# Kernel tuning notes

Hardware: AMD Instinct MI355X
Metric: run time of the kernel (lower is better)

Reference implementation:

```python
import jax, jax.numpy as jnp
import numpy as np

PAD = 3            # ConstantPad1d padding
PAD_VAL = -1.0     # ConstantPad1d value
STRIDE = 1
POOL = 2           # pool_size == pool_stride == 2
BN_EPS = 1e-5


def setup_inputs() -> dict:
    key = jax.random.key(0)
    k1, k2 = jax.random.split(key)
    x = jax.random.normal(k1, (256, 64, 4096), dtype=jnp.float32)
    W = jax.random.normal(k2, (128, 64, 7), dtype=jnp.float32)
    alpha = jnp.ones((1,), dtype=jnp.float32) * 0.25   # nn.PReLU default init
    gamma = jnp.ones((128,), dtype=jnp.float32)
    beta = jnp.zeros((128,), dtype=jnp.float32)
    return {"x": x, "W": W, "alpha": alpha, "gamma": gamma, "beta": beta}


def reference(x, W, alpha, gamma, beta):
    # 1) constant pad with value PAD_VAL along length
    xp = jnp.pad(x, ((0, 0), (0, 0), (PAD, PAD)), constant_values=PAD_VAL)
    # 2) binarize activations and weights (sign; sign(0)=0 as in torch)
    ba = jnp.sign(xp)
    bw = jnp.sign(W)
    # 3) float conv1d on +/-1 values, no bias  -> [B, Cout, L]
    y = jax.lax.conv_general_dilated(
        ba, bw, window_strides=(STRIDE,), padding='VALID',
        dimension_numbers=('NCW', 'OIW', 'NCW'))
    # 4) max pool k=2, s=2 (non-overlapping -> reshape trick)
    B, C, L = y.shape
    y = y[:, :, : (L // POOL) * POOL].reshape(B, C, L // POOL, POOL).max(axis=-1)
    # 5) PReLU with single shared alpha
    y = jnp.where(y > 0, y, alpha[0] * y)
    # 6) BatchNorm1d in training mode: batch stats over (B, L), biased variance
    mean = jnp.mean(y, axis=(0, 2), keepdims=True)
    var = jnp.mean((y - mean) ** 2, axis=(0, 2), keepdims=True)
    y = (y - mean) * jax.lax.rsqrt(var + BN_EPS)
    y = y * gamma[None, :, None] + beta[None, :, None]
    return y
```

## Files before the change

### kernel.cpp

```cpp
#include <hip/hip_runtime.h>
#include <stdint.h>

#define BATCH 256
#define CIN   64
#define LIN   4096
#define PADN  3
#define LPAD  4102
#define COUT  128
#define KW    7
#define LPOOL 2048
#define NBUCKET 64
#define NPERCH (256LL * 2048LL)

typedef unsigned long long u64;
typedef __attribute__((ext_vector_type(4)))  int i32x4;
typedef __attribute__((ext_vector_type(16))) int i32x16;
typedef __attribute__((ext_vector_type(8)))  short s16x8;

#define ACC_ZERO {0,0,0,0,0,0,0,0,0,0,0,0,0,0,0,0}

__global__ __launch_bounds__(256) void pack_x_kernel(const float* __restrict__ x,
                                                     char* __restrict__ sx,
                                                     int b_base)
{
    const int t  = threadIdx.x;
    const int lt = blockIdx.x;
    const int bl = blockIdx.y;
    const int b  = b_base + bl;
    const int l  = lt * 256 + t;
    const float* xb = x + (size_t)b * CIN * LIN + l;

    int o[16];
    #pragma unroll
    for (int cw = 0; cw < 16; ++cw) {
        unsigned wv = 0;
        #pragma unroll
        for (int j = 0; j < 4; ++j) {
            float v = xb[(size_t)(cw * 4 + j) * LIN];
            unsigned s = (v > 0.0f) ? 1u : ((v < 0.0f) ? 0xFFu : 0u);
            wv |= s << (8 * j);
        }
        o[cw] = (int)wv;
    }
    i32x4* dst = (i32x4*)(sx + ((size_t)bl * LPAD + (l + PADN)) * 64);
    dst[0] = (i32x4){o[0],  o[1],  o[2],  o[3]};
    dst[1] = (i32x4){o[4],  o[5],  o[6],  o[7]};
    dst[2] = (i32x4){o[8],  o[9],  o[10], o[11]};
    dst[3] = (i32x4){o[12], o[13], o[14], o[15]};

    const i32x4 ff = (i32x4){-1, -1, -1, -1};
    if (lt == 0 && t < PADN) {
        i32x4* pd = (i32x4*)(sx + ((size_t)bl * LPAD + t) * 64);
        pd[0] = ff; pd[1] = ff; pd[2] = ff; pd[3] = ff;
    }
    if (lt == 15 && t < PADN) {
        i32x4* pd = (i32x4*)(sx + ((size_t)bl * LPAD + (LIN + PADN) + t) * 64);
        pd[0] = ff; pd[1] = ff; pd[2] = ff; pd[3] = ff;
    }
}

__global__ __launch_bounds__(256) void pack_w_kernel(const float* __restrict__ w,
                                                     char* __restrict__ pwb)
{
    int idx = blockIdx.x * 256 + threadIdx.x;
    if (idx >= KW * COUT * CIN) return;
    int kk = idx >> 13;
    int co = (idx >> 6) & 127;
    int c  = idx & 63;
    float v = w[((size_t)co * CIN + c) * KW + kk];
    pwb[idx] = (char)((v > 0.0f) ? 1 : ((v < 0.0f) ? -1 : 0));
}

template<int STOREP>
__global__ __launch_bounds__(256, 3) void conv_stats_kernel(
    const char* __restrict__ sx, const char* __restrict__ pwb,
    u64* __restrict__ stats, short* __restrict__ pstore, int b_base)
{
    const int tid  = threadIdx.x;
    const int lane = tid & 63;
    const int w    = tid >> 6;
    const int ngrp = w & 1;
    const int mgrp = w >> 1;
    const int col  = lane & 31;
    const int hi   = lane >> 5;
    const int bl   = blockIdx.y;
    const int mchunk = blockIdx.x;

    const char* sxb = sx + (size_t)bl * LPAD * 64;
    const char* wb0 = pwb + (size_t)((ngrp * 64 + col) * 64) + hi * 16;

    const int gb = b_base + bl;
    short* prow0 = STOREP ? (pstore + ((size_t)gb * COUT + ngrp * 64 + col) * LPOOL)
                          : (short*)nullptr;
    short* prow1 = STOREP ? (prow0 + (size_t)32 * LPOOL) : (short*)nullptr;

    int sp0=0, sn0=0, qp0=0, qn0=0, sp1=0, sn1=0, qp1=0, qn1=0;

    for (int mt = 0; mt < 4; ++mt) {
        const int q0 = mchunk * 256 + mgrp * 128 + mt * 32;
        i32x16 acc0 = ACC_ZERO, acc1 = ACC_ZERO;
        #pragma unroll
        for (int kk = 0; kk < KW; ++kk) {
            const char* ar = sxb + (size_t)(q0 + col + kk) * 64;
            i32x4 x0 = *(const i32x4*)(ar + hi * 16);
            i32x4 x1 = *(const i32x4*)(ar + 32 + hi * 16);
            const char* wk = wb0 + (size_t)kk * (COUT * 64);
            i32x4 w00 = *(const i32x4*)(wk);
            i32x4 w01 = *(const i32x4*)(wk + 32);
            i32x4 w10 = *(const i32x4*)(wk + 2048);
            i32x4 w11 = *(const i32x4*)(wk + 2048 + 32);
            acc0 = __builtin_amdgcn_mfma_i32_32x32x32_i8(x0, w00, acc0, 0, 0, 0);
            acc0 = __builtin_amdgcn_mfma_i32_32x32x32_i8(x1, w01, acc0, 0, 0, 0);
            acc1 = __builtin_amdgcn_mfma_i32_32x32x32_i8(x0, w10, acc1, 0, 0, 0);
            acc1 = __builtin_amdgcn_mfma_i32_32x32x32_i8(x1, w11, acc1, 0, 0, 0);
        }
        const int lp0 = q0 >> 1;
        #pragma unroll
        for (int r = 0; r < 8; ++r) {
            int p = acc0[2*r] > acc0[2*r+1] ? acc0[2*r] : acc0[2*r+1];
            int q = p * p;
            bool pos = p > 0;
            sp0 += pos ? p : 0;  sn0 += pos ? 0 : p;
            qp0 += pos ? q : 0;  qn0 += pos ? 0 : q;
            int p1 = acc1[2*r] > acc1[2*r+1] ? acc1[2*r] : acc1[2*r+1];
            int q1 = p1 * p1;
            bool pos1 = p1 > 0;
            sp1 += pos1 ? p1 : 0;  sn1 += pos1 ? 0 : p1;
            qp1 += pos1 ? q1 : 0;  qn1 += pos1 ? 0 : q1;
            if (STOREP) {
                const int prow = (r & 1) + 4 * (r >> 1) + 2 * hi;
                prow0[lp0 + prow] = (short)p;
                prow1[lp0 + prow] = (short)p1;
            }
        }
    }

    sp0 += __shfl_xor(sp0, 32);  sn0 += __shfl_xor(sn0, 32);
    qp0 += __shfl_xor(qp0, 32);  qn0 += __shfl_xor(qn0, 32);
    sp1 += __shfl_xor(sp1, 32);  sn1 += __shfl_xor(sn1, 32);
    qp1 += __shfl_xor(qp1, 32);  qn1 += __shfl_xor(qn1, 32);

    if (hi == 0) {
        const int bkt = gb & (NBUCKET - 1);
        u64* s0 = stats + (size_t)(bkt * COUT + ngrp * 64 + col) * 4;
        atomicAdd(&s0[0], (u64)(long long)sp0);
        atomicAdd(&s0[1], (u64)(long long)sn0);
        atomicAdd(&s0[2], (u64)(long long)qp0);
        atomicAdd(&s0[3], (u64)(long long)qn0);
        u64* s1 = stats + (size_t)(bkt * COUT + ngrp * 64 + 32 + col) * 4;
        atomicAdd(&s1[0], (u64)(long long)sp1);
        atomicAdd(&s1[1], (u64)(long long)sn1);
        atomicAdd(&s1[2], (u64)(long long)qp1);
        atomicAdd(&s1[3], (u64)(long long)qn1);
    }
}

__global__ void finalize_kernel(const u64* __restrict__ stats,
                                const float* __restrict__ alpha,
                                const float* __restrict__ gamma,
                                const float* __restrict__ beta,
                                float2* __restrict__ scsh)
{
    int c = threadIdx.x;
    if (c >= COUT) return;
    long long s[4] = {0, 0, 0, 0};
    for (int bk = 0; bk < NBUCKET; ++bk)
        #pragma unroll
        for (int i = 0; i < 4; ++i)
            s[i] += (long long)stats[(size_t)(bk * COUT + c) * 4 + i];
    double a    = (double)alpha[0];
    double N    = (double)NPERCH;
    double sum  = (double)s[0] + a * (double)s[1];
    double ssq  = (double)s[2] + a * a * (double)s[3];
    double mean = sum / N;
    double var  = ssq / N - mean * mean;
    double inv  = 1.0 / sqrt(var + 1e-5);
    double g    = (double)gamma[c];
    scsh[c] = make_float2((float)(g * inv),
                          (float)((double)beta[c] - mean * g * inv));
}

__global__ __launch_bounds__(256) void bn_write_kernel(
    const short* __restrict__ p, const float2* __restrict__ scsh,
    const float* __restrict__ alpha, float* __restrict__ out)
{
    const float a = alpha[0];
    const size_t i = ((size_t)blockIdx.x * 256 + threadIdx.x) * 8;
    const int co = (int)((i >> 11) & (COUT - 1));
    const float2 ss = scsh[co];
    const s16x8 v = *(const s16x8*)(p + i);
    float4 o0, o1;
    #pragma unroll
    for (int j = 0; j < 4; ++j) {
        float pv = (float)v[j];
        float y = (pv > 0.0f) ? pv : a * pv;
        ((float*)&o0)[j] = fmaf(y, ss.x, ss.y);
    }
    #pragma unroll
    for (int j = 0; j < 4; ++j) {
        float pv = (float)v[4 + j];
        float y = (pv > 0.0f) ? pv : a * pv;
        ((float*)&o1)[j] = fmaf(y, ss.x, ss.y);
    }
    *(float4*)(out + i)     = o0;
    *(float4*)(out + i + 4) = o1;
}

__global__ __launch_bounds__(256, 2) void conv_write_kernel(
    const char* __restrict__ sx, const char* __restrict__ pwb,
    const float2* __restrict__ scsh, const float* __restrict__ alpha,
    float* __restrict__ out, int b_base)
{
    const int tid  = threadIdx.x;
    const int lane = tid & 63;
    const int w    = tid >> 6;
    const int ngrp = w & 1;
    const int mgrp = w >> 1;
    const int col  = lane & 31;
    const int hi   = lane >> 5;
    const int bl   = blockIdx.y;
    const int mchunk = blockIdx.x;

    const char* sxb = sx + (size_t)bl * LPAD * 64;
    const char* wb0 = pwb + (size_t)((ngrp * 64 + col) * 64) + hi * 16;

    const float a = alpha[0];
    const float2 ss0 = scsh[ngrp * 64 + col];
    const float2 ss1 = scsh[ngrp * 64 + 32 + col];
    const int gb = b_base + bl;
    float* orow0 = out + ((size_t)gb * COUT + ngrp * 64 + col) * LPOOL;
    float* orow1 = orow0 + (size_t)32 * LPOOL;

    for (int mt = 0; mt < 4; ++mt) {
        const int q0 = mchunk * 256 + mgrp * 128 + mt * 32;
        i32x16 a00 = ACC_ZERO, a01 = ACC_ZERO, a10 = ACC_ZERO, a11 = ACC_ZERO;
        #pragma unroll
        for (int kk = 0; kk < KW; ++kk) {
            const char* ar = sxb + (size_t)(q0 + col + kk) * 64;
            i32x4 x0 = *(const i32x4*)(ar + hi * 16);
            i32x4 x1 = *(const i32x4*)(ar + 32 + hi * 16);
            const char* wk = wb0 + (size_t)kk * (COUT * 64);
            i32x4 w00 = *(const i32x4*)(wk);
            i32x4 w01 = *(const i32x4*)(wk + 32);
            i32x4 w10 = *(const i32x4*)(wk + 2048);
            i32x4 w11 = *(const i32x4*)(wk + 2048 + 32);
            a00 = __builtin_amdgcn_mfma_i32_32x32x32_i8(x0, w00, a00, 0, 0, 0);
            a01 = __builtin_amdgcn_mfma_i32_32x32x32_i8(x1, w01, a01, 0, 0, 0);
            a10 = __builtin_amdgcn_mfma_i32_32x32x32_i8(x0, w10, a10, 0, 0, 0);
            a11 = __builtin_amdgcn_mfma_i32_32x32x32_i8(x1, w11, a11, 0, 0, 0);
        }
        i32x16 acc0 = a00 + a01;
        i32x16 acc1 = a10 + a11;
        const int lp0 = q0 >> 1;
        #pragma unroll
        for (int r = 0; r < 8; ++r) {
            const int prow = (r & 1) + 4 * (r >> 1) + 2 * hi;
            int p = acc0[2*r] > acc0[2*r+1] ? acc0[2*r] : acc0[2*r+1];
            float y = (p > 0) ? (float)p : a * (float)p;
            orow0[lp0 + prow] = fmaf(y, ss0.x, ss0.y);
            p = acc1[2*r] > acc1[2*r+1] ? acc1[2*r] : acc1[2*r+1];
            y = (p > 0) ? (float)p : a * (float)p;
            orow1[lp0 + prow] = fmaf(y, ss1.x, ss1.y);
        }
    }
}

extern "C" void kernel_launch(void* const* d_in, const int* in_sizes, int n_in,
                              void* d_out, int out_size, void* d_ws, size_t ws_size,
                              hipStream_t stream)
{
    const float* x     = (const float*)d_in[0];
    const float* W     = (const float*)d_in[1];
    const float* alpha = (const float*)d_in[2];
    const float* gamma = (const float*)d_in[3];
    const float* beta  = (const float*)d_in[4];
    float* out = (float*)d_out;

    const size_t sx_sz    = (size_t)BATCH * LPAD * 64;
    const size_t p_sz     = (size_t)BATCH * COUT * LPOOL * 2;
    const size_t pwb_sz   = (size_t)KW * COUT * CIN;
    const size_t stats_sz = (size_t)NBUCKET * COUT * 4 * 8;
    const size_t scsh_sz  = (size_t)COUT * 8;
    const size_t fixed    = pwb_sz + stats_sz + scsh_sz + 4096;

    char* ws = (char*)d_ws;

    if (ws_size >= sx_sz + p_sz + fixed) {
        char* sx = ws;
        size_t off = (sx_sz + 255) & ~(size_t)255;
        short* p = (short*)(ws + off);       off = (off + p_sz + 255) & ~(size_t)255;
        char* pwb = ws + off;                off = (off + pwb_sz + 255) & ~(size_t)255;
        u64* stats = (u64*)(ws + off);       off = (off + stats_sz + 255) & ~(size_t)255;
        float2* scsh = (float2*)(ws + off);

        hipMemsetAsync(stats, 0, stats_sz, stream);
        pack_w_kernel<<<dim3(224), 256, 0, stream>>>(W, pwb);
        pack_x_kernel<<<dim3(16, BATCH), 256, 0, stream>>>(x, sx, 0);
        conv_stats_kernel<1><<<dim3(16, BATCH), 256, 0, stream>>>(sx, pwb, stats, p, 0);
        finalize_kernel<<<dim3(1), 128, 0, stream>>>(stats, alpha, gamma, beta, scsh);
        bn_write_kernel<<<dim3(32768), 256, 0, stream>>>(p, scsh, alpha, out);
        return;
    }

    const size_t PER_B = (size_t)LPAD * 64;
    int nb = BATCH;
    if (ws_size < PER_B * BATCH + fixed) {
        size_t avail = (ws_size > fixed) ? (ws_size - fixed) : PER_B;
        nb = (int)(avail / PER_B);
        if (nb < 1) nb = 1;
        if (nb > BATCH) nb = BATCH;
    }

    char* sx = ws;
    size_t off = ((PER_B * (size_t)nb) + 255) & ~(size_t)255;
    char* pwb = ws + off;               off = (off + pwb_sz + 255) & ~(size_t)255;
    u64* stats = (u64*)(ws + off);      off = (off + stats_sz + 255) & ~(size_t)255;
    float2* scsh = (float2*)(ws + off);

    hipMemsetAsync(stats, 0, stats_sz, stream);
    pack_w_kernel<<<dim3(224), 256, 0, stream>>>(W, pwb);

    for (int b0 = 0; b0 < BATCH; b0 += nb) {
        int n = (BATCH - b0 < nb) ? (BATCH - b0) : nb;
        pack_x_kernel<<<dim3(16, n), 256, 0, stream>>>(x, sx, b0);
        conv_stats_kernel<0><<<dim3(16, n), 256, 0, stream>>>(sx, pwb, stats, nullptr, b0);
    }
    finalize_kernel<<<dim3(1), 128, 0, stream>>>(stats, alpha, gamma, beta, scsh);

    if (nb == BATCH) {
        conv_write_kernel<<<dim3(16, BATCH), 256, 0, stream>>>(sx, pwb, scsh, alpha, out, 0);
    } else {
        for (int b0 = 0; b0 < BATCH; b0 += nb) {
            int n = (BATCH - b0 < nb) ? (BATCH - b0) : nb;
            pack_x_kernel<<<dim3(16, n), 256, 0, stream>>>(x, sx, b0);
            conv_write_kernel<<<dim3(16, n), 256, 0, stream>>>(sx, pwb, scsh, alpha, out, b0);
        }
    }
}
```

Before: 388.4 us.

## Store pooled conv tiles in MFMA-native layout with vectorized packed writes

The stats kernel previously scattered 2-byte short stores into a row-major [B,Cout,L] intermediate, giving poorly coalesced writes. It now packs each lane's eight pooled values into one 16-byte store, laid out in per-wave MFMA fragment order. The BN write kernel is restructured to read that tiled layout, rebuild the logical positions and emit float4 output rows. This costs more complex indexing in the consumer, and its reads and writes may be less contiguous per thread.

```diff
diff --git a/kernel.cpp b/kernel.cpp
--- a/kernel.cpp
+++ b/kernel.cpp
@@ -19,6 +19,11 @@
 
 #define ACC_ZERO {0,0,0,0,0,0,0,0,0,0,0,0,0,0,0,0}
 
+static __device__ __forceinline__ int pk16(int a, int b)
+{
+    return (a & 0xFFFF) | (b << 16);
+}
+
 __global__ __launch_bounds__(256) void pack_x_kernel(const float* __restrict__ x,
                                                      char* __restrict__ sx,
                                                      int b_base)
@@ -90,9 +95,9 @@
     const char* wb0 = pwb + (size_t)((ngrp * 64 + col) * 64) + hi * 16;
 
     const int gb = b_base + bl;
-    short* prow0 = STOREP ? (pstore + ((size_t)gb * COUT + ngrp * 64 + col) * LPOOL)
-                          : (short*)nullptr;
-    short* prow1 = STOREP ? (prow0 + (size_t)32 * LPOOL) : (short*)nullptr;
+    short* pwave = STOREP
+        ? (pstore + ((((size_t)gb * 16 + mchunk) * 4 + w) * 2) * 4 * 64 * 8)
+        : (short*)nullptr;
 
     int sp0=0, sn0=0, qp0=0, qn0=0, sp1=0, sn1=0, qp1=0, qn1=0;
 
@@ -114,24 +119,32 @@
             acc1 = __builtin_amdgcn_mfma_i32_32x32x32_i8(x0, w10, acc1, 0, 0, 0);
             acc1 = __builtin_amdgcn_mfma_i32_32x32x32_i8(x1, w11, acc1, 0, 0, 0);
         }
-        const int lp0 = q0 >> 1;
+
+        int v0[8], v1[8];
         #pragma unroll
         for (int r = 0; r < 8; ++r) {
-            int p = acc0[2*r] > acc0[2*r+1] ? acc0[2*r] : acc0[2*r+1];
-            int q = p * p;
+            v0[r] = acc0[2*r] > acc0[2*r+1] ? acc0[2*r] : acc0[2*r+1];
+            v1[r] = acc1[2*r] > acc1[2*r+1] ? acc1[2*r] : acc1[2*r+1];
+        }
+        #pragma unroll
+        for (int r = 0; r < 8; ++r) {
+            int p = v0[r], q = p * p;
             bool pos = p > 0;
             sp0 += pos ? p : 0;  sn0 += pos ? 0 : p;
             qp0 += pos ? q : 0;  qn0 += pos ? 0 : q;
-            int p1 = acc1[2*r] > acc1[2*r+1] ? acc1[2*r] : acc1[2*r+1];
-            int q1 = p1 * p1;
+            int p1 = v1[r], q1 = p1 * p1;
             bool pos1 = p1 > 0;
             sp1 += pos1 ? p1 : 0;  sn1 += pos1 ? 0 : p1;
             qp1 += pos1 ? q1 : 0;  qn1 += pos1 ? 0 : q1;
-            if (STOREP) {
-                const int prow = (r & 1) + 4 * (r >> 1) + 2 * hi;
-                prow0[lp0 + prow] = (short)p;
-                prow1[lp0 + prow] = (short)p1;
-            }
+        }
+
+        if (STOREP) {
+            i32x4 o0 = (i32x4){pk16(v0[0], v0[1]), pk16(v0[2], v0[3]),
+                               pk16(v0[4], v0[5]), pk16(v0[6], v0[7])};
+            *(i32x4*)(pwave + ((size_t)(mt * 64 + lane)) * 8) = o0;
+            i32x4 o1 = (i32x4){pk16(v1[0], v1[1]), pk16(v1[2], v1[3]),
+                               pk16(v1[4], v1[5]), pk16(v1[6], v1[7])};
+            *(i32x4*)(pwave + ((size_t)((4 + mt) * 64 + lane)) * 8) = o1;
         }
     }
 
@@ -184,26 +197,38 @@
     const short* __restrict__ p, const float2* __restrict__ scsh,
     const float* __restrict__ alpha, float* __restrict__ out)
 {
+    const int mchunk = blockIdx.x;
+    const int b      = blockIdx.y;
     const float a = alpha[0];
-    const size_t i = ((size_t)blockIdx.x * 256 + threadIdx.x) * 8;
-    const int co = (int)((i >> 11) & (COUT - 1));
-    const float2 ss = scsh[co];
-    const s16x8 v = *(const s16x8*)(p + i);
-    float4 o0, o1;
+    const short* ptile = p + (((size_t)b * 16 + mchunk) * 4) * 2 * 4 * 64 * 8;
+
     #pragma unroll
-    for (int j = 0; j < 4; ++j) {
-        float pv = (float)v[j];
-        float y = (pv > 0.0f) ? pv : a * pv;
-        ((float*)&o0)[j] = fmaf(y, ss.x, ss.y);
-    }
-    #pragma unroll
-    for (int j = 0; j < 4; ++j) {
-        float pv = (float)v[4 + j];
-        float y = (pv > 0.0f) ? pv : a * pv;
-        ((float*)&o1)[j] = fmaf(y, ss.x, ss.y);
-    }
-    *(float4*)(out + i)     = o0;
-    *(float4*)(out + i + 4) = o1;
+    for (int i = 0; i < 4; ++i) {
+        const int item = i * 256 + threadIdx.x;
+        const int cout = item >> 3;
+        const int seg  = item & 7;
+        const int mgrp = seg >> 2, mt = seg & 3;
+        const int wv   = mgrp * 2 + (cout >> 6);
+        const int chain = (cout >> 5) & 1;
+        const int col   = cout & 31;
+
+        const short* base = ptile + ((size_t)((wv * 2 + chain) * 4 + mt) * 64) * 8;
+        s16x8 b0 = *(const s16x8*)(base + (size_t)col * 8);
+        s16x8 b1 = *(const s16x8*)(base + (size_t)(32 + col) * 8);
+
+        const float2 ss = scsh[cout];
+        float* op = out + ((size_t)b * COUT + cout) * LPOOL + mchunk * 128 + seg * 16;
+        #pragma unroll
+        for (int q = 0; q < 4; ++q) {
+            float4 o;
+            float pv, y;
+            pv = (float)b0[2*q];     y = (pv > 0.0f) ? pv : a * pv;  o.x = fmaf(y, ss.x, ss.y);
+            pv = (float)b0[2*q + 1]; y = (pv > 0.0f) ? pv : a * pv;  o.y = fmaf(y, ss.x, ss.y);
+            pv = (float)b1[2*q];     y = (pv > 0.0f) ? pv : a * pv;  o.z = fmaf(y, ss.x, ss.y);
+            pv = (float)b1[2*q + 1]; y = (pv > 0.0f) ? pv : a * pv;  o.w = fmaf(y, ss.x, ss.y);
+            *(float4*)(op + q * 4) = o;
+        }
+    }
 }
 
 __global__ __launch_bounds__(256, 2) void conv_write_kernel(
@@ -298,7 +323,7 @@
         pack_x_kernel<<<dim3(16, BATCH), 256, 0, stream>>>(x, sx, 0);
         conv_stats_kernel<1><<<dim3(16, BATCH), 256, 0, stream>>>(sx, pwb, stats, p, 0);
         finalize_kernel<<<dim3(1), 128, 0, stream>>>(stats, alpha, gamma, beta, scsh);
-        bn_write_kernel<<<dim3(32768), 256, 0, stream>>>(p, scsh, alpha, out);
+        bn_write_kernel<<<dim3(16, BATCH), 256, 0, stream>>>(p, scsh, alpha, out);
         return;
     }
 
```

Result: faster. 365.2 us (-6.0%).
